# Performance work log

Hardware: AMD Instinct MI355X
Metric: run time of the kernel (lower is better)

Reference implementation:

```python
import jax, jax.numpy as jnp
import numpy as np

B, S, T, H, E, VIN, VOUT = 2048, 24, 25, 256, 300, 64, 128


def gru_cell(x, h, Wih, Whh, bih, bhh):
    # PyTorch GRU gate order: r, z, n
    gi = x @ Wih + bih          # [B, 3H]
    gh = h @ Whh + bhh          # [B, 3H]
    hd = h.shape[-1]
    ir, iz, in_ = gi[:, :hd], gi[:, hd:2 * hd], gi[:, 2 * hd:]
    hr, hz, hn = gh[:, :hd], gh[:, hd:2 * hd], gh[:, 2 * hd:]
    r = jax.nn.sigmoid(ir + hr)
    z = jax.nn.sigmoid(iz + hz)
    n = jnp.tanh(in_ + r * hn)
    return (1.0 - z) * n + z * h


def setup_inputs() -> dict:
    key = jax.random.key(0)
    ks = jax.random.split(key, 26)
    it = iter(range(26))

    def p(shape):
        return jax.random.normal(ks[next(it)], shape, jnp.float32) * 0.05

    src = jax.random.randint(ks[next(it)], (S, B), 0, VIN)
    trg = jax.random.randint(ks[next(it)], (T, B), 0, VOUT)
    return dict(
        src=src, trg=trg,
        enc_emb=p((VIN, E)),
        enc_Wih_f=p((E, 3 * H)), enc_Whh_f=p((H, 3 * H)), enc_bih_f=p((3 * H,)), enc_bhh_f=p((3 * H,)),
        enc_Wih_b=p((E, 3 * H)), enc_Whh_b=p((H, 3 * H)), enc_bih_b=p((3 * H,)), enc_bhh_b=p((3 * H,)),
        enc_fcW=p((2 * H, H)), enc_fcb=p((H,)),
        attn_Wh=p((H, H)), attn_We=p((2 * H, H)), attn_b=p((H,)), attn_v=p((H,)),
        dec_emb=p((VOUT, E)),
        dec_Wih=p((E + 2 * H, 3 * H)), dec_Whh=p((H, 3 * H)), dec_bih=p((3 * H,)), dec_bhh=p((3 * H,)),
        fcW=p((H + 2 * H + E, VOUT)), fcb=p((VOUT,)),
        teacher_forcing_ratio=1,
    )


def reference(src, trg, enc_emb, enc_Wih_f, enc_Whh_f, enc_bih_f, enc_bhh_f,
              enc_Wih_b, enc_Whh_b, enc_bih_b, enc_bhh_b, enc_fcW, enc_fcb,
              attn_Wh, attn_We, attn_b, attn_v, dec_emb,
              dec_Wih, dec_Whh, dec_bih, dec_bhh, fcW, fcb,
              teacher_forcing_ratio):
    # ---- Encoder: bidirectional single-layer GRU ----
    x = enc_emb[src]                                   # [S, B, E]
    h0 = jnp.zeros((x.shape[1], H), x.dtype)

    def mk(Wih, Whh, bih, bhh):
        def step(h, xt):
            hn = gru_cell(xt, h, Wih, Whh, bih, bhh)
            return hn, hn
        return step

    hf, out_f = jax.lax.scan(mk(enc_Wih_f, enc_Whh_f, enc_bih_f, enc_bhh_f), h0, x)
    hb, out_b = jax.lax.scan(mk(enc_Wih_b, enc_Whh_b, enc_bih_b, enc_bhh_b), h0, x[::-1])
    enc_out = jnp.concatenate([out_f, out_b[::-1]], axis=-1)   # [S, B, 2H]
    hidden = jnp.tanh(jnp.concatenate([hf, hb], axis=-1) @ enc_fcW + enc_fcb)  # [B, H]

    # ---- Decoder: teacher-forced loop (teacher_forcing_ratio=1 => deterministic) ----
    enc_bse = enc_out.transpose(1, 0, 2)               # [B, S, 2H]
    enc_proj = enc_bse @ attn_We                       # [B, S, H] (hoisted linear part of attn)
    embed_seq = dec_emb[trg[:-1]]                      # [T-1, B, E]

    def dec_step(h, emb_t):
        energy = jnp.tanh((h @ attn_Wh)[:, None, :] + enc_proj + attn_b)  # [B, S, H]
        a = jax.nn.softmax(energy @ attn_v, axis=-1)                      # [B, S]
        weighted = jnp.einsum('bs,bsd->bd', a, enc_bse)                   # [B, 2H]
        xg = jnp.concatenate([emb_t, weighted], axis=-1)                  # [B, E+2H]
        hn = gru_cell(xg, h, dec_Wih, dec_Whh, dec_bih, dec_bhh)          # [B, H]
        logits = jnp.concatenate([hn, weighted, emb_t], axis=-1) @ fcW + fcb
        return hn, logits

    _, logits = jax.lax.scan(dec_step, hidden, embed_seq)  # [T-1, B, VOUT]
    outputs = jnp.concatenate(
        [jnp.zeros((1,) + logits.shape[1:], logits.dtype), logits], axis=0)  # [T, B, VOUT]
    return outputs
```

## Files before the change

### kernel.cpp

```cpp
#include <hip/hip_runtime.h>
#include <hip/hip_bf16.h>

typedef __hip_bfloat16 bf16;
typedef __attribute__((ext_vector_type(8))) short short8;
typedef __attribute__((ext_vector_type(4))) short short4v;
typedef __attribute__((ext_vector_type(4))) float f32x4;

#define MFMA(va, vb, vc) \
  __builtin_amdgcn_mfma_f32_16x16x32_bf16(va, vb, vc, 0, 0, 0)

__device__ __forceinline__ float to_f(float x) { return x; }
__device__ __forceinline__ float to_f(bf16 x) { return __bfloat162float(x); }
__device__ __forceinline__ float ldp(const void* p, size_t i, bool f32) {
  return f32 ? ((const float*)p)[i] : __bfloat162float(((const bf16*)p)[i]);
}
__device__ __forceinline__ short f2b(float f) {
  bf16 h = __float2bfloat16(f);
  return *reinterpret_cast<short*>(&h);
}
__device__ __forceinline__ float b2f(short s_) {
  unsigned int ui = ((unsigned int)(unsigned short)s_) << 16;
  float f;
  __builtin_memcpy(&f, &ui, 4);
  return f;
}
__device__ __forceinline__ int perm1024(int c) {
  return ((c & 255) >> 4) * 64 + (c >> 8) * 16 + (c & 15);
}

__global__ void detect_kernel(const void* __restrict__ probe,
                              unsigned* __restrict__ flag) {
  __shared__ int sbad;
  if (threadIdx.x == 0) sbad = 0;
  __syncthreads();
  const unsigned short* u = (const unsigned short*)probe;
  int bad = 0;
  for (int i = threadIdx.x; i < 2048; i += 256) {
    unsigned short w = u[i];
    unsigned e = (w >> 7) & 0xFFu;
    bool plaus = (w == 0) || (w == 0x8000u) || (e >= 0x60u && e <= 0x7Eu);
    if (!plaus) bad++;
  }
  atomicAdd(&sbad, bad);
  __syncthreads();
  if (threadIdx.x == 0) *flag = (sbad > 100) ? 1u : 0u;
}

#define MAXSEG 24
struct PrepArgs {
  int nseg;
  const void* src[MAXSEG];
  long long soff[MAXSEG];
  short* dst[MAXSEG];
  int scols[MAXSEG];
  int dstride[MAXSEG];
  int transp[MAXSEG];
  long long prefix[MAXSEG + 1];
};
__global__ void prep_kernel(PrepArgs a, const unsigned* __restrict__ dflag) {
  const bool isf32 = (*dflag != 0u);
  long long i = (long long)blockIdx.x * 256 + threadIdx.x;
  if (i >= a.prefix[a.nseg]) return;
  int s = 0;
  while (i >= a.prefix[s + 1]) s++;
  long long loc = i - a.prefix[s];
  long long r = loc / a.scols[s], c = loc % a.scols[s];
  float v = a.src[s] ? ldp(a.src[s], (size_t)(a.soff[s] + loc), isf32) : 0.f;
  int tp = a.transp[s];
  long long idx;
  if (tp == 1)
    idx = c * a.dstride[s] + r;
  else if (tp == 2)
    idx = (long long)perm1024((int)c) * a.dstride[s] + r;
  else if (tp == 3)
    idx = perm1024((int)c);
  else
    idx = r * a.dstride[s] + c;
  a.dst[s][idx] = f2b(v);
}

struct GJob {
  const bf16* A;
  const short* WT;
  const bf16* bias;
  float* Cf;
  bf16* Ch;
  const float* Cin;
  const int* cinrow;
  int lda, wst, K, M, N, flags;
};
struct GJobs {
  GJob j[4];
};

__global__ __launch_bounds__(256) void mj_gemm(GJobs args) {
  GJob jb = args.j[blockIdx.z];
  const int n0 = blockIdx.x * 128, m0 = blockIdx.y * 128;
  if (n0 >= jb.N || m0 >= jb.M) return;
  __shared__ short As[128][40];
  __shared__ short Bs[128][40];
  const int tid = threadIdx.x, lane = tid & 63, wave = tid >> 6;
  const int srow = tid >> 1, skoff = (tid & 1) * 16;
  const int wr = (wave >> 1) * 64, wc = (wave & 1) * 64;

  const short* abase =
      (const short*)jb.A + (long long)(m0 + srow) * jb.lda + skoff;
  const short* bbase = jb.WT + (long long)(n0 + srow) * jb.wst + skoff;
  f32x4 acc[4][4];
#pragma unroll
  for (int i = 0; i < 4; i++)
#pragma unroll
    for (int j = 0; j < 4; j++) acc[i][j] = 0.f;

  short8 a0 = *(const short8*)(abase);
  short8 a1 = *(const short8*)(abase + 8);
  short8 b0 = *(const short8*)(bbase);
  short8 b1 = *(const short8*)(bbase + 8);
  for (int k0 = 0; k0 < jb.K; k0 += 32) {
    __syncthreads();
    *(short8*)&As[srow][skoff] = a0;
    *(short8*)&As[srow][skoff + 8] = a1;
    *(short8*)&Bs[srow][skoff] = b0;
    *(short8*)&Bs[srow][skoff + 8] = b1;
    __syncthreads();
    int kn = (k0 + 32 < jb.K) ? k0 + 32 : k0;
    a0 = *(const short8*)(abase + kn);
    a1 = *(const short8*)(abase + kn + 8);
    b0 = *(const short8*)(bbase + kn);
    b1 = *(const short8*)(bbase + kn + 8);
    short8 af[4], bfr[4];
#pragma unroll
    for (int i = 0; i < 4; i++)
      af[i] = *(short8*)&As[wr + i * 16 + (lane & 15)][(lane >> 4) * 8];
#pragma unroll
    for (int j = 0; j < 4; j++)
      bfr[j] = *(short8*)&Bs[wc + j * 16 + (lane & 15)][(lane >> 4) * 8];
#pragma unroll
    for (int i = 0; i < 4; i++)
#pragma unroll
      for (int j = 0; j < 4; j++) acc[i][j] = MFMA(af[i], bfr[j], acc[i][j]);
  }
  const int N = jb.N;
  const float* cin = jb.Cin;
  const int* cri = jb.cinrow;
#pragma unroll
  for (int j = 0; j < 4; j++) {
    int col = n0 + wc + j * 16 + (lane & 15);
    float bv = jb.bias ? to_f(jb.bias[col]) : 0.f;
#pragma unroll
    for (int i = 0; i < 4; i++) {
#pragma unroll
      for (int r = 0; r < 4; r++) {
        int row = m0 + wr + i * 16 + (lane >> 4) * 4 + r;
        float v = acc[i][j][r] + bv;
        if (cin) {
          long long crow = cri ? (long long)cri[row] : (long long)row;
          v += cin[crow * N + col];
        }
        if (jb.flags & 4) v = tanhf(v);
        if (jb.Cf) jb.Cf[(long long)row * N + col] = v;
        if (jb.Ch) jb.Ch[(long long)row * N + col] = __float2bfloat16(v);
      }
    }
  }
}

struct CJob {
  const bf16* A;
  const short* WT;
  const bf16* bias;
  const int* tok;
  const bf16* giTab;
  float* hF;
  bf16* hBf;
  bf16* out2;
  long long out2s;
  int lda, wst, K, hstride, hoff;
};
struct CJobs {
  CJob j[2];
};

__global__ __launch_bounds__(256) void mj_gemm_cell(CJobs args) {
  CJob jb = args.j[blockIdx.z];
  const int n0 = blockIdx.x * 128, m0 = blockIdx.y * 128;
  __shared__ short As[128][40];
  __shared__ short Bs[128][40];
  __shared__ int toks[128];
  const int tid = threadIdx.x, lane = tid & 63, wave = tid >> 6;
  const int srow = tid >> 1, skoff = (tid & 1) * 16;
  const int wr = (wave >> 1) * 64, wcq = (wave & 1) * 64;

  if (tid < 128) toks[tid] = jb.tok[m0 + tid];
  const short* abase =
      (const short*)jb.A + (long long)(m0 + srow) * jb.lda + skoff;
  const short* bbase = jb.WT + (long long)(n0 + srow) * jb.wst + skoff;

  f32x4 acc[4][4];
#pragma unroll
  for (int i = 0; i < 4; i++)
#pragma unroll
    for (int j = 0; j < 4; j++) acc[i][j] = 0.f;

  short8 a0 = *(const short8*)(abase);
  short8 a1 = *(const short8*)(abase + 8);
  short8 b0 = *(const short8*)(bbase);
  short8 b1 = *(const short8*)(bbase + 8);
  for (int k0 = 0; k0 < jb.K; k0 += 32) {
    __syncthreads();
    *(short8*)&As[srow][skoff] = a0;
    *(short8*)&As[srow][skoff + 8] = a1;
    *(short8*)&Bs[srow][skoff] = b0;
    *(short8*)&Bs[srow][skoff + 8] = b1;
    __syncthreads();
    int kn = (k0 + 32 < jb.K) ? k0 + 32 : k0;
    a0 = *(const short8*)(abase + kn);
    a1 = *(const short8*)(abase + kn + 8);
    b0 = *(const short8*)(bbase + kn);
    b1 = *(const short8*)(bbase + kn + 8);
    short8 af[4], bfr[4];
#pragma unroll
    for (int i = 0; i < 4; i++)
      af[i] = *(short8*)&As[wr + i * 16 + (lane & 15)][(lane >> 4) * 8];
#pragma unroll
    for (int j = 0; j < 4; j++)
      bfr[j] = *(short8*)&Bs[wcq + j * 16 + (lane & 15)][(lane >> 4) * 8];
#pragma unroll
    for (int i = 0; i < 4; i++)
#pragma unroll
      for (int j = 0; j < 4; j++) acc[i][j] = MFMA(af[i], bfr[j], acc[i][j]);
  }

  const int u = lane & 15, hi4 = (lane >> 4) * 4;
  const int i_h = ((n0 + wcq) >> 6) * 16 + u;
  const float b0g = to_f(jb.bias[n0 + wcq + u]);
  const float b1g = to_f(jb.bias[n0 + wcq + 16 + u]);
  const float b2g = to_f(jb.bias[n0 + wcq + 32 + u]);
#pragma unroll
  for (int i = 0; i < 4; i++) {
#pragma unroll
    for (int r = 0; r < 4; r++) {
      int row = m0 + wr + i * 16 + hi4 + r;
      const bf16* gi = jb.giTab + (long long)toks[row - m0] * 768 + i_h;
      float ir = to_f(gi[0]), iz = to_f(gi[256]), in_ = to_f(gi[512]);
      float hr = acc[i][0][r] + b0g;
      float hz = acc[i][1][r] + b1g;
      float hn = acc[i][2][r] + b2g;
      long long hidx = (long long)row * jb.hstride + jb.hoff + i_h;
      float hv = jb.hF[hidx];
      float rr = 1.f / (1.f + expf(-(ir + hr)));
      float zz = 1.f / (1.f + expf(-(iz + hz)));
      float nn = tanhf(in_ + rr * hn);
      float o = (1.f - zz) * nn + zz * hv;
      jb.hF[hidx] = o;
      jb.hBf[hidx] = __float2bfloat16(o);
      jb.out2[(long long)row * jb.out2s + i_h] = __float2bfloat16(o);
    }
  }
}

struct A3Args {
  const bf16* ghw;
  const bf16* proj;
  const bf16* bse;
  const void* v;
  const unsigned* dflag;
  bf16* xr;
};
__global__ __launch_bounds__(256) void attn3_kernel(A3Args a) {
  const int b = blockIdx.x, tid = threadIdx.x;
  const int wave = tid >> 6, lane = tid & 63;
  __shared__ float esc[24];
  __shared__ float aw[24];
  const bool isf32 = (*a.dflag != 0u);
  float vv[4], hw[4];
  {
    short4v h4 = *(const short4v*)((const short*)a.ghw + (size_t)b * 1280 +
                                   1024 + lane * 4);
#pragma unroll
    for (int e = 0; e < 4; e++) {
      hw[e] = b2f(h4[e]);
      vv[e] = ldp(a.v, lane * 4 + e, isf32);
    }
  }
  const short* pb = (const short*)a.proj + (size_t)b * 6144 + lane * 4;
  short4v p4s[6];
#pragma unroll
  for (int i = 0; i < 6; i++)
    p4s[i] = *(const short4v*)(pb + (wave * 6 + i) * 256);
#pragma unroll
  for (int i = 0; i < 6; i++) {
    float t = 0.f;
#pragma unroll
    for (int e = 0; e < 4; e++)
      t += vv[e] * tanhf(hw[e] + b2f(p4s[i][e]));
#pragma unroll
    for (int off = 1; off < 64; off <<= 1) t += __shfl_xor(t, off, 64);
    if (lane == 0) esc[wave * 6 + i] = t;
  }
  __syncthreads();
  if (wave == 0) {
    float xv = (lane < 24) ? esc[lane] : -1e30f;
    float mx = xv;
#pragma unroll
    for (int off = 1; off < 64; off <<= 1)
      mx = fmaxf(mx, __shfl_xor(mx, off, 64));
    float e = (lane < 24) ? expf(xv - mx) : 0.f;
    float sm = e;
#pragma unroll
    for (int off = 1; off < 64; off <<= 1) sm += __shfl_xor(sm, off, 64);
    if (lane < 24) aw[lane] = e / sm;
  }
  __syncthreads();
  const short* eb = (const short*)a.bse + (size_t)b * 12288 + tid * 2;
  float w0 = 0.f, w1 = 0.f;
#pragma unroll
  for (int s = 0; s < 24; s++) {
    unsigned q = *(const unsigned*)(eb + s * 512);
    float aa = aw[s];
    w0 += aa * b2f((short)(q & 0xffff));
    w1 += aa * b2f((short)(q >> 16));
  }
  unsigned o = ((unsigned)(unsigned short)f2b(w1) << 16) |
               (unsigned)(unsigned short)f2b(w0);
  *(unsigned*)((short*)a.xr + (size_t)b * 768 + tid * 2) = o;
}

struct C3Args {
  const bf16* xr;
  const bf16* ghw;
  const short* W7p;
  const bf16* bhhP;
  const int* tok;
  const bf16* giTabE;
  float* hF;
  bf16* hnext;
  bf16* xout;
};

__global__ __launch_bounds__(256) void cell3_kernel(C3Args a) {
  const int n0 = blockIdx.x * 128, m0 = blockIdx.y * 128;
  __shared__ short As[128][40];
  __shared__ short Bs[128][40];
  __shared__ int toks[128];
  const int tid = threadIdx.x, lane = tid & 63, wave = tid >> 6;
  const int srow = tid >> 1, skoff = (tid & 1) * 16;
  const int wr = (wave >> 1) * 64, wcq = (wave & 1) * 64;
  if (tid < 128) toks[tid] = a.tok[m0 + tid];

  f32x4 acc[4][3];
#pragma unroll
  for (int i = 0; i < 4; i++)
#pragma unroll
    for (int j = 0; j < 3; j++) acc[i][j] = 0.f;

  {
    const short* abase =
        (const short*)a.xr + (long long)(m0 + srow) * 768 + skoff;
    const short* bbase = a.W7p + (long long)(n0 + srow) * 512 + skoff;
    short8 a0 = *(const short8*)(abase);
    short8 a1 = *(const short8*)(abase + 8);
    short8 b0 = *(const short8*)(bbase);
    short8 b1 = *(const short8*)(bbase + 8);
    for (int k0 = 0; k0 < 512; k0 += 32) {
      __syncthreads();
      *(short8*)&As[srow][skoff] = a0;
      *(short8*)&As[srow][skoff + 8] = a1;
      *(short8*)&Bs[srow][skoff] = b0;
      *(short8*)&Bs[srow][skoff + 8] = b1;
      __syncthreads();
      int kn = (k0 + 32 < 512) ? k0 + 32 : k0;
      a0 = *(const short8*)(abase + kn);
      a1 = *(const short8*)(abase + kn + 8);
      b0 = *(const short8*)(bbase + kn);
      b1 = *(const short8*)(bbase + kn + 8);
      short8 af[4], bfr[3];
#pragma unroll
      for (int i = 0; i < 4; i++)
        af[i] = *(short8*)&As[wr + i * 16 + (lane & 15)][(lane >> 4) * 8];
#pragma unroll
      for (int j = 0; j < 3; j++)
        bfr[j] = *(short8*)&Bs[wcq + j * 16 + (lane & 15)][(lane >> 4) * 8];
#pragma unroll
      for (int i = 0; i < 4; i++)
#pragma unroll
        for (int j = 0; j < 3; j++) acc[i][j] = MFMA(af[i], bfr[j], acc[i][j]);
    }
  }

  const int u = lane & 15, hi4 = (lane >> 4) * 4;
  const int i_h = ((n0 + wcq) >> 6) * 16 + u;
  const float b0g = to_f(a.bhhP[n0 + wcq + u]);
  const float b1g = to_f(a.bhhP[n0 + wcq + 16 + u]);
  const float b2g = to_f(a.bhhP[n0 + wcq + 32 + u]);
#pragma unroll
  for (int i = 0; i < 4; i++) {
#pragma unroll
    for (int r = 0; r < 4; r++) {
      int row = m0 + wr + i * 16 + hi4 + r;
      const bf16* gi = a.giTabE + (long long)toks[row - m0] * 768 + i_h;
      const bf16* gb = a.ghw + (long long)row * 1280 + (n0 + wcq) + u;
      float ir = acc[i][0][r] + to_f(gi[0]);
      float iz = acc[i][1][r] + to_f(gi[256]);
      float in_ = acc[i][2][r] + to_f(gi[512]);
      float hr = to_f(gb[0]) + b0g;
      float hz = to_f(gb[16]) + b1g;
      float hn = to_f(gb[32]) + b2g;
      long long hidx = (long long)row * 256 + i_h;
      float hv = a.hF[hidx];
      float rr = 1.f / (1.f + expf(-(ir + hr)));
      float zz = 1.f / (1.f + expf(-(iz + hz)));
      float nn = tanhf(in_ + rr * hn);
      float o = (1.f - zz) * nn + zz * hv;
      a.hF[hidx] = o;
      a.hnext[hidx] = __float2bfloat16(o);
      a.xout[(long long)row * 768 + 512 + i_h] = __float2bfloat16(o);
    }
  }
}

__global__ void sentinel_kernel(float* out, int n) {
  int i = blockIdx.x * 256 + threadIdx.x;
  if (i < n) out[i] = 123.0f;
}

extern "C" void kernel_launch(void* const* d_in, const int* in_sizes, int n_in,
                              void* d_out, int out_size, void* d_ws,
                              size_t ws_size, hipStream_t stream) {
  const int B = 2048, S = 24, T = 25, VOUT = 128;
  const int* src = (const int*)d_in[0];
  const int* trg = (const int*)d_in[1];
  const void* enc_emb = d_in[2];
  const void* enc_Wih_f = d_in[3];
  const void* enc_Whh_f = d_in[4];
  const void* enc_bih_f = d_in[5];
  const void* enc_bhh_f = d_in[6];
  const void* enc_Wih_b = d_in[7];
  const void* enc_Whh_b = d_in[8];
  const void* enc_bih_b = d_in[9];
  const void* enc_bhh_b = d_in[10];
  const void* enc_fcW = d_in[11];
  const void* enc_fcb = d_in[12];
  const void* attn_Wh = d_in[13];
  const void* attn_We = d_in[14];
  const void* attn_b = d_in[15];
  const void* attn_v = d_in[16];
  const void* dec_emb = d_in[17];
  const void* dec_Wih = d_in[18];
  const void* dec_Whh = d_in[19];
  const void* dec_bih = d_in[20];
  const void* dec_bhh = d_in[21];
  const void* fcW = d_in[22];
  const void* fcb = d_in[23];
  float* out = (float*)d_out;

  size_t need = 0;
  auto place = [&](size_t bytes) {
    size_t off = need;
    need += (bytes + 255) & ~(size_t)255;
    return off;
  };
  size_t o_flag = place(256);
  size_t o_wstart = need;
  size_t oEmbE = place(64 * 320 * 2);
  size_t oEmbD = place(128 * 320 * 2);
  size_t oWT1 = place(768 * 320 * 2);
  size_t oWT2 = place(1024 * 256 * 2);
  size_t oWT3 = place(768 * 320 * 2);
  size_t oWT4 = place(1024 * 256 * 2);
  size_t oWT5 = place(256 * 512 * 2);
  size_t oWT6 = place(256 * 512 * 2);
  size_t oWcK = place(1280 * 256 * 2);
  size_t oW7aT = place(768 * 320 * 2);
  size_t oW7bT = place(1024 * 512 * 2);
  size_t oW8aT = place(128 * 320 * 2);
  size_t oW8bT = place(128 * 768 * 2);
  size_t oB1 = place(768 * 2), oB2 = place(1024 * 2);
  size_t oB3 = place(768 * 2), oB4 = place(1024 * 2);
  size_t oB5 = place(256 * 2), oB6 = place(256 * 2);
  size_t oB7 = place(768 * 2), oBcP = place(1024 * 2), oB8 = place(128 * 2);
  size_t o_wend = need;
  size_t o_bse = place((size_t)B * S * 512 * 2);
  size_t o_proj = place((size_t)B * S * 256 * 2);
  size_t o_xgc = place((size_t)(T - 1) * B * 768 * 2);
  size_t o_hfb = place((size_t)B * 512 * 4);
  size_t o_hb0 = place((size_t)B * 512 * 2);
  size_t o_hb1 = place((size_t)B * 512 * 2);
  size_t o_hd = place((size_t)B * 256 * 4);
  size_t o_hdb0 = place((size_t)B * 256 * 2);
  size_t o_hdb1 = place((size_t)B * 256 * 2);
  size_t o_ghw = place((size_t)B * 1280 * 2);
  size_t o_gtF = place(128 * 768 * 2);
  size_t o_gtB = place(128 * 768 * 2);
  size_t o_gtE = place(128 * 768 * 2);
  size_t o_fcT = place(128 * 128 * 4);

  if (ws_size < need) {
    sentinel_kernel<<<(out_size + 255) / 256, 256, 0, stream>>>(out, out_size);
    return;
  }

  char* base = (char*)d_ws;
  unsigned* dflag = (unsigned*)(base + o_flag);
  bf16* embE = (bf16*)(base + oEmbE);
  bf16* embD = (bf16*)(base + oEmbD);
  short* WT1 = (short*)(base + oWT1);
  short* WT2p = (short*)(base + oWT2);
  short* WT3 = (short*)(base + oWT3);
  short* WT4p = (short*)(base + oWT4);
  short* WT5 = (short*)(base + oWT5);
  short* WT6 = (short*)(base + oWT6);
  short* WcK = (short*)(base + oWcK);
  short* W7aT = (short*)(base + oW7aT);
  short* W7bTp = (short*)(base + oW7bT);
  short* W8aT = (short*)(base + oW8aT);
  short* W8bT = (short*)(base + oW8bT);
  bf16 *B1 = (bf16*)(base + oB1), *B2p = (bf16*)(base + oB2);
  bf16 *B3 = (bf16*)(base + oB3), *B4p = (bf16*)(base + oB4);
  bf16 *B5 = (bf16*)(base + oB5), *B6 = (bf16*)(base + oB6);
  bf16 *B7 = (bf16*)(base + oB7), *BcP = (bf16*)(base + oBcP);
  bf16* B8 = (bf16*)(base + oB8);
  bf16* bse = (bf16*)(base + o_bse);
  bf16* proj = (bf16*)(base + o_proj);
  bf16* xgcAll = (bf16*)(base + o_xgc);
  float* hfb = (float*)(base + o_hfb);
  bf16* hb[2] = {(bf16*)(base + o_hb0), (bf16*)(base + o_hb1)};
  float* h_d = (float*)(base + o_hd);
  bf16* hdbf[2] = {(bf16*)(base + o_hdb0), (bf16*)(base + o_hdb1)};
  bf16* ghw = (bf16*)(base + o_ghw);
  bf16* giTabF = (bf16*)(base + o_gtF);
  bf16* giTabB = (bf16*)(base + o_gtB);
  bf16* giTabE = (bf16*)(base + o_gtE);
  float* fcTab = (float*)(base + o_fcT);

  detect_kernel<<<1, 256, 0, stream>>>(enc_emb, dflag);
  (void)hipMemsetAsync(base + o_wstart, 0, o_wend - o_wstart, stream);

  PrepArgs pa;
  int ns = 0;
  long long tot = 0;
  auto seg = [&](const void* s, long long soff, short* dst, int scols,
                 int dstride, int transp, long long count) {
    pa.src[ns] = s;
    pa.soff[ns] = soff;
    pa.dst[ns] = dst;
    pa.scols[ns] = scols;
    pa.dstride[ns] = dstride;
    pa.transp[ns] = transp;
    pa.prefix[ns] = tot;
    tot += count;
    ns++;
  };
  seg(enc_emb, 0, (short*)embE, 300, 320, 0, 64 * 300);
  seg(dec_emb, 0, (short*)embD, 300, 320, 0, 128 * 300);
  seg(enc_Wih_f, 0, WT1, 768, 320, 1, 230400);
  seg(enc_Whh_f, 0, WT2p, 768, 256, 2, 196608);
  seg(enc_Wih_b, 0, WT3, 768, 320, 1, 230400);
  seg(enc_Whh_b, 0, WT4p, 768, 256, 2, 196608);
  seg(enc_fcW, 0, WT5, 256, 512, 1, 131072);
  seg(attn_We, 0, WT6, 256, 512, 1, 131072);
  seg(dec_Whh, 0, WcK, 768, 256, 2, 196608);
  seg(attn_Wh, 0, WcK + 1024 * 256, 256, 256, 1, 65536);
  seg(dec_Wih, 0, W7aT, 768, 320, 1, 300 * 768);
  seg(dec_Wih, (long long)300 * 768, W7bTp, 768, 512, 2, 512 * 768);
  seg(fcW, (long long)768 * 128, W8aT, 128, 320, 1, 300 * 128);
  seg(fcW, (long long)256 * 128, W8bT, 128, 768, 1, 512 * 128);
  seg(fcW, 0, W8bT + 512, 128, 768, 1, 256 * 128);
  seg(enc_bih_f, 0, (short*)B1, 768, 768, 0, 768);
  seg(enc_bhh_f, 0, (short*)B2p, 768, 1024, 3, 768);
  seg(enc_bih_b, 0, (short*)B3, 768, 768, 0, 768);
  seg(enc_bhh_b, 0, (short*)B4p, 768, 1024, 3, 768);
  seg(enc_fcb, 0, (short*)B5, 256, 256, 0, 256);
  seg(attn_b, 0, (short*)B6, 256, 256, 0, 256);
  seg(dec_bih, 0, (short*)B7, 768, 768, 0, 768);
  seg(dec_bhh, 0, (short*)BcP, 768, 1024, 3, 768);
  seg(fcb, 0, (short*)B8, 128, 128, 0, 128);
  pa.prefix[ns] = tot;
  pa.nseg = ns;
  prep_kernel<<<(int)((tot + 255) / 256), 256, 0, stream>>>(pa, dflag);

  (void)hipMemsetAsync(hfb, 0, (size_t)B * 512 * 4, stream);
  (void)hipMemsetAsync(hb[0], 0, (size_t)B * 512 * 2, stream);
  (void)hipMemsetAsync(out, 0, (size_t)B * VOUT * 4, stream);

  auto launch = [&](const GJob* jobs, int nj, int gx, int gy) {
    GJobs a{};
    for (int i = 0; i < nj; i++) a.j[i] = jobs[i];
    mj_gemm<<<dim3(gx, gy, nj), 256, 0, stream>>>(a);
  };

  {
    GJob tj[4];
    tj[0] = {embE, WT1, B1, nullptr, giTabF, nullptr, nullptr,
             320, 320, 320, 128, 768, 0};
    tj[1] = {embE, WT3, B3, nullptr, giTabB, nullptr, nullptr,
             320, 320, 320, 128, 768, 0};
    tj[2] = {embD, W7aT, B7, nullptr, giTabE, nullptr, nullptr,
             320, 320, 320, 128, 768, 0};
    tj[3] = {embD, W8aT, B8, fcTab, nullptr, nullptr, nullptr,
             320, 320, 320, 128, 128, 0};
    launch(tj, 4, 6, 1);
  }

  for (int s = 0; s < S; s++) {
    CJobs ca{};
    ca.j[0] = {hb[s & 1], WT2p, B2p, src + (size_t)s * B, giTabF,
               hfb, hb[(s + 1) & 1], bse + (size_t)s * 512, 12288,
               512, 256, 256, 512, 0};
    ca.j[1] = {hb[s & 1] + 256, WT4p, B4p, src + (size_t)(S - 1 - s) * B,
               giTabB, hfb, hb[(s + 1) & 1],
               bse + (size_t)(S - 1 - s) * 512 + 256, 12288,
               512, 256, 256, 512, 256};
    mj_gemm_cell<<<dim3(8, 16, 2), 256, 0, stream>>>(ca);
  }

  {
    GJob mj[2];
    mj[0] = {hb[0], WT5, B5, h_d, hdbf[0], nullptr, nullptr,
             512, 512, 512, B, 256, 4};
    mj[1] = {bse, WT6, B6, nullptr, proj, nullptr, nullptr,
             512, 512, 512, B * S, 256, 0};
    launch(mj, 2, 2, 384);
  }

  for (int t = 0; t < T - 1; t++) {
    bf16* xr = xgcAll + (size_t)t * B * 768;
    GJob jw = {hdbf[t & 1], WcK, nullptr, nullptr, ghw, nullptr, nullptr,
               256, 256, 256, B, 1280, 0};
    launch(&jw, 1, 10, 16);
    A3Args aa{ghw, proj, bse, attn_v, dflag, xr};
    attn3_kernel<<<B, 256, 0, stream>>>(aa);
    C3Args cc{xr, ghw, W7bTp, BcP, trg + (size_t)t * B, giTabE,
              h_d, hdbf[(t + 1) & 1], xr};
    cell3_kernel<<<dim3(8, 16), 256, 0, stream>>>(cc);
  }

  {
    GJob jf = {xgcAll, W8bT, nullptr, out + (size_t)B * VOUT, nullptr,
               fcTab, trg, 768, 768, 768, (T - 1) * B, 128, 0};
    launch(&jf, 1, 1, 384);
  }
}
```

Measured before the change: 1.794 ms.

## Split decoder hidden GEMM and fuse Whh part into attention kernel launch

The per-step decoder GEMM that computed both h@Whh and h@attn_Wh (1280 columns) is split. Only the small h@attn_Wh projection (256 columns) stays as a separate launch ahead of attention. The h@Whh GEMM (1024 columns) now runs as 128 extra blocks appended to the attention kernel's grid, so it executes alongside attention instead of serially before it. This adds shared memory to every attention block, which may reduce occupancy, and adds a hand-written MFMA GEMM path.

```diff
diff --git a/kernel.cpp b/kernel.cpp
--- a/kernel.cpp
+++ b/kernel.cpp
@@ -259,24 +259,85 @@
   }
 }
 
-struct A3Args {
-  const bf16* ghw;
+struct AGArgs {
+  const bf16* hwh;
   const bf16* proj;
   const bf16* bse;
   const void* v;
   const unsigned* dflag;
   bf16* xr;
+  const bf16* hdbf;
+  const short* WhhP;
+  bf16* ghw;
 };
-__global__ __launch_bounds__(256) void attn3_kernel(A3Args a) {
-  const int b = blockIdx.x, tid = threadIdx.x;
-  const int wave = tid >> 6, lane = tid & 63;
+__global__ __launch_bounds__(256) void attng_kernel(AGArgs a) {
+  const int tid = threadIdx.x, wave = tid >> 6, lane = tid & 63;
+  __shared__ short As[128][40];
+  __shared__ short Bs[128][40];
   __shared__ float esc[24];
   __shared__ float aw[24];
+  const int bid = blockIdx.x;
+  if (bid >= 2048) {
+    const int gid = bid - 2048;
+    const int n0 = (gid & 7) * 128, m0 = (gid >> 3) * 128;
+    const int srow = tid >> 1, skoff = (tid & 1) * 16;
+    const int wr = (wave >> 1) * 64, wcq = (wave & 1) * 64;
+    f32x4 acc[4][3];
+#pragma unroll
+    for (int i = 0; i < 4; i++)
+#pragma unroll
+      for (int j = 0; j < 3; j++) acc[i][j] = 0.f;
+    const short* abase =
+        (const short*)a.hdbf + (long long)(m0 + srow) * 256 + skoff;
+    const short* bbase = a.WhhP + (long long)(n0 + srow) * 256 + skoff;
+    short8 a0 = *(const short8*)(abase);
+    short8 a1 = *(const short8*)(abase + 8);
+    short8 b0 = *(const short8*)(bbase);
+    short8 b1 = *(const short8*)(bbase + 8);
+    for (int k0 = 0; k0 < 256; k0 += 32) {
+      __syncthreads();
+      *(short8*)&As[srow][skoff] = a0;
+      *(short8*)&As[srow][skoff + 8] = a1;
+      *(short8*)&Bs[srow][skoff] = b0;
+      *(short8*)&Bs[srow][skoff + 8] = b1;
+      __syncthreads();
+      int kn = (k0 + 32 < 256) ? k0 + 32 : k0;
+      a0 = *(const short8*)(abase + kn);
+      a1 = *(const short8*)(abase + kn + 8);
+      b0 = *(const short8*)(bbase + kn);
+      b1 = *(const short8*)(bbase + kn + 8);
+      short8 af[4], bfr[3];
+#pragma unroll
+      for (int i = 0; i < 4; i++)
+        af[i] = *(short8*)&As[wr + i * 16 + (lane & 15)][(lane >> 4) * 8];
+#pragma unroll
+      for (int j = 0; j < 3; j++)
+        bfr[j] = *(short8*)&Bs[wcq + j * 16 + (lane & 15)][(lane >> 4) * 8];
+#pragma unroll
+      for (int i = 0; i < 4; i++)
+#pragma unroll
+        for (int j = 0; j < 3; j++) acc[i][j] = MFMA(af[i], bfr[j], acc[i][j]);
+    }
+    const int u = lane & 15, hi4 = (lane >> 4) * 4;
+#pragma unroll
+    for (int j = 0; j < 3; j++) {
+      const int col = n0 + wcq + j * 16 + u;
+#pragma unroll
+      for (int i = 0; i < 4; i++)
+#pragma unroll
+        for (int r = 0; r < 4; r++) {
+          int row = m0 + wr + i * 16 + hi4 + r;
+          a.ghw[(long long)row * 1024 + col] = __float2bfloat16(acc[i][j][r]);
+        }
+    }
+    return;
+  }
+  const int b = bid;
   const bool isf32 = (*a.dflag != 0u);
   float vv[4], hw[4];
   {
-    short4v h4 = *(const short4v*)((const short*)a.ghw + (size_t)b * 1280 +
-                                   1024 + lane * 4);
+    short4v h4 =
+        *(const short4v*)((const short*)a.hwh + (size_t)b * 256 + lane * 4);
 #pragma unroll
     for (int e = 0; e < 4; e++) {
       hw[e] = b2f(h4[e]);
@@ -399,7 +460,7 @@
     for (int r = 0; r < 4; r++) {
       int row = m0 + wr + i * 16 + hi4 + r;
       const bf16* gi = a.giTabE + (long long)toks[row - m0] * 768 + i_h;
-      const bf16* gb = a.ghw + (long long)row * 1280 + (n0 + wcq) + u;
+      const bf16* gb = a.ghw + (long long)row * 1024 + (n0 + wcq) + u;
       float ir = acc[i][0][r] + to_f(gi[0]);
       float iz = acc[i][1][r] + to_f(gi[256]);
       float in_ = acc[i][2][r] + to_f(gi[512]);
@@ -470,7 +531,8 @@
   size_t oWT4 = place(1024 * 256 * 2);
   size_t oWT5 = place(256 * 512 * 2);
   size_t oWT6 = place(256 * 512 * 2);
-  size_t oWcK = place(1280 * 256 * 2);
+  size_t oWhhP = place(1024 * 256 * 2);
+  size_t oWhT = place(256 * 256 * 2);
   size_t oW7aT = place(768 * 320 * 2);
   size_t oW7bT = place(1024 * 512 * 2);
   size_t oW8aT = place(128 * 320 * 2);
@@ -489,7 +551,8 @@
   size_t o_hd = place((size_t)B * 256 * 4);
   size_t o_hdb0 = place((size_t)B * 256 * 2);
   size_t o_hdb1 = place((size_t)B * 256 * 2);
-  size_t o_ghw = place((size_t)B * 1280 * 2);
+  size_t o_hwh = place((size_t)B * 256 * 2);
+  size_t o_ghw = place((size_t)B * 1024 * 2);
   size_t o_gtF = place(128 * 768 * 2);
   size_t o_gtB = place(128 * 768 * 2);
   size_t o_gtE = place(128 * 768 * 2);
@@ -510,7 +573,8 @@
   short* WT4p = (short*)(base + oWT4);
   short* WT5 = (short*)(base + oWT5);
   short* WT6 = (short*)(base + oWT6);
-  short* WcK = (short*)(base + oWcK);
+  short* WhhP = (short*)(base + oWhhP);
+  short* WhT = (short*)(base + oWhT);
   short* W7aT = (short*)(base + oW7aT);
   short* W7bTp = (short*)(base + oW7bT);
   short* W8aT = (short*)(base + oW8aT);
@@ -527,6 +591,7 @@
   bf16* hb[2] = {(bf16*)(base + o_hb0), (bf16*)(base + o_hb1)};
   float* h_d = (float*)(base + o_hd);
   bf16* hdbf[2] = {(bf16*)(base + o_hdb0), (bf16*)(base + o_hdb1)};
+  bf16* hwh = (bf16*)(base + o_hwh);
   bf16* ghw = (bf16*)(base + o_ghw);
   bf16* giTabF = (bf16*)(base + o_gtF);
   bf16* giTabB = (bf16*)(base + o_gtB);
@@ -559,8 +624,8 @@
   seg(enc_Whh_b, 0, WT4p, 768, 256, 2, 196608);
   seg(enc_fcW, 0, WT5, 256, 512, 1, 131072);
   seg(attn_We, 0, WT6, 256, 512, 1, 131072);
-  seg(dec_Whh, 0, WcK, 768, 256, 2, 196608);
-  seg(attn_Wh, 0, WcK + 1024 * 256, 256, 256, 1, 65536);
+  seg(dec_Whh, 0, WhhP, 768, 256, 2, 196608);
+  seg(attn_Wh, 0, WhT, 256, 256, 1, 65536);
   seg(dec_Wih, 0, W7aT, 768, 320, 1, 300 * 768);
   seg(dec_Wih, (long long)300 * 768, W7bTp, 768, 512, 2, 512 * 768);
   seg(fcW, (long long)768 * 128, W8aT, 128, 320, 1, 300 * 128);
@@ -625,11 +690,12 @@
 
   for (int t = 0; t < T - 1; t++) {
     bf16* xr = xgcAll + (size_t)t * B * 768;
-    GJob jw = {hdbf[t & 1], WcK, nullptr, nullptr, ghw, nullptr, nullptr,
-               256, 256, 256, B, 1280, 0};
-    launch(&jw, 1, 10, 16);
-    A3Args aa{ghw, proj, bse, attn_v, dflag, xr};
-    attn3_kernel<<<B, 256, 0, stream>>>(aa);
+    GJob jh = {hdbf[t & 1], WhT, nullptr, nullptr, hwh, nullptr, nullptr,
+               256, 256, 256, B, 256, 0};
+    launch(&jh, 1, 2, 16);
+    AGArgs aa{hwh, proj, bse, attn_v, dflag, xr,
+              hdbf[t & 1], WhhP, ghw};
+    attng_kernel<<<2048 + 128, 256, 0, stream>>>(aa);
     C3Args cc{xr, ghw, W7bTp, BcP, trg + (size_t)t * B, giTabE,
               h_d, hdbf[(t + 1) & 1], xr};
     cell3_kernel<<<dim3(8, 16), 256, 0, stream>>>(cc);
```

Measured after the change: 1.986 ms. 1.11x slower.
